# Kernel optimization log

Hardware: AMD Instinct MI355X
Metric: run time of the kernel (lower is better)

## Reference

```python
import jax, jax.numpy as jnp
import numpy as np

EMBED = 1024
HEADS = 16
HEAD_DIM = EMBED // HEADS
HIDDEN = 4 * EMBED
EPS = 1e-5


def setup_inputs() -> dict:
    key = jax.random.key(0)
    ks = jax.random.split(key, 9)
    s = lambda fan_in: 1.0 / np.sqrt(fan_in)
    inp = {
        "x": jax.random.normal(ks[0], (2, 2048, EMBED), dtype=jnp.float32),
        "ln1_w": jnp.ones((EMBED,), jnp.float32),
        "ln1_b": jnp.zeros((EMBED,), jnp.float32),
        "ln2_w": jnp.ones((EMBED,), jnp.float32),
        "ln2_b": jnp.zeros((EMBED,), jnp.float32),
        "qkv_w": jax.random.uniform(ks[1], (EMBED, 3 * EMBED), jnp.float32, -s(EMBED), s(EMBED)),
        "qkv_b": jax.random.uniform(ks[2], (3 * EMBED,), jnp.float32, -s(EMBED), s(EMBED)),
        "proj_w": jax.random.uniform(ks[3], (EMBED, EMBED), jnp.float32, -s(EMBED), s(EMBED)),
        "proj_b": jax.random.uniform(ks[4], (EMBED,), jnp.float32, -s(EMBED), s(EMBED)),
        "fc1_w": jax.random.uniform(ks[5], (EMBED, HIDDEN), jnp.float32, -s(EMBED), s(EMBED)),
        "fc1_b": jax.random.uniform(ks[6], (HIDDEN,), jnp.float32, -s(EMBED), s(EMBED)),
        "fc2_w": jax.random.uniform(ks[7], (HIDDEN, EMBED), jnp.float32, -s(HIDDEN), s(HIDDEN)),
        "fc2_b": jax.random.uniform(ks[8], (EMBED,), jnp.float32, -s(HIDDEN), s(HIDDEN)),
    }
    return inp


def _layernorm(x, w, b):
    mu = jnp.mean(x, axis=-1, keepdims=True)
    var = jnp.mean(jnp.square(x - mu), axis=-1, keepdims=True)
    return (x - mu) * jax.lax.rsqrt(var + EPS) * w + b


def _attn(x, qkv_w, qkv_b, proj_w, proj_b):
    B, N, C = x.shape
    qkv = x @ qkv_w + qkv_b                      # [B,N,3C]
    qkv = qkv.reshape(B, N, 3, HEADS, HEAD_DIM)
    q, k, v = qkv[:, :, 0], qkv[:, :, 1], qkv[:, :, 2]   # [B,N,H,D]
    scale = HEAD_DIM ** -0.5
    scores = jnp.einsum("bqhd,bkhd->bhqk", q, k) * scale  # [B,H,N,N]
    attn = jax.nn.softmax(scores, axis=-1)
    out = jnp.einsum("bhqk,bkhd->bqhd", attn, v).reshape(B, N, C)
    return out @ proj_w + proj_b


def _mlp(x, fc1_w, fc1_b, fc2_w, fc2_b):
    h = jax.nn.gelu(x @ fc1_w + fc1_b, approximate=False)
    return h @ fc2_w + fc2_b


def reference(x, ln1_w, ln1_b, ln2_w, ln2_b, qkv_w, qkv_b, proj_w, proj_b,
              fc1_w, fc1_b, fc2_w, fc2_b):
    # pre-norm transformer block (eval mode: dropout/drop_path are identity)
    x = x + _attn(_layernorm(x, ln1_w, ln1_b), qkv_w, qkv_b, proj_w, proj_b)
    x = x + _mlp(_layernorm(x, ln2_w, ln2_b), fc1_w, fc1_b, fc2_w, fc2_b)
    return x
```

## Files before the change

### kernel.cpp

```cpp
#include <hip/hip_runtime.h>
#include <hip/hip_bf16.h>

#define SEQ    2048
#define BATCH  2
#define MTOK   4096
#define EMBED  1024
#define HEADS  16
#define HDIM   64
#define QKV3   3072
#define FFN    4096

typedef __attribute__((ext_vector_type(8))) short bf16x8;
typedef __attribute__((ext_vector_type(4))) float f32x4;

static __device__ __forceinline__ unsigned short f2bf(float f) {
  union { float f; unsigned u; } x; x.f = f;
  unsigned r = x.u + 0x7FFFu + ((x.u >> 16) & 1u);
  return (unsigned short)(r >> 16);
}
static __device__ __forceinline__ float bf2f(unsigned short u) {
  union { unsigned u; float f; } x; x.u = ((unsigned)u) << 16; return x.f;
}
static __device__ __forceinline__ unsigned pk2bf(float a, float b) {
#if __has_builtin(__builtin_amdgcn_cvt_pk_bf16_f32)
  typedef __attribute__((ext_vector_type(2))) __bf16 bf16x2_t;
  union { bf16x2_t v; unsigned u; } x;
  x.v = __builtin_amdgcn_cvt_pk_bf16_f32(a, b);
  return x.u;
#else
  return ((unsigned)f2bf(a)) | (((unsigned)f2bf(b)) << 16);
#endif
}
static __device__ __forceinline__ float fexp2(float x) {
#if __has_builtin(__builtin_amdgcn_exp2f)
  return __builtin_amdgcn_exp2f(x);
#else
  return exp2f(x);
#endif
}

static __device__ __forceinline__ void gload16(const unsigned short* g, unsigned short* l) {
  __builtin_amdgcn_global_load_lds((const __attribute__((address_space(1))) void*)g,
                                   (__attribute__((address_space(3))) void*)l, 16, 0, 0);
}

struct TD { const float* W; unsigned short* T; int K, N, ntx, base; };
struct TD4 { TD d[4]; };

__global__ void transpose_all(TD4 td) {
  __shared__ float t[32][33];
  int bid = blockIdx.x;
  int i = 0;
  if (bid >= td.d[1].base) i = 1;
  if (bid >= td.d[2].base) i = 2;
  if (bid >= td.d[3].base) i = 3;
  const TD& D = td.d[i];
  int local = bid - D.base;
  int n0 = (local % D.ntx) * 32, k0 = (local / D.ntx) * 32;
  int tx = threadIdx.x, ty = threadIdx.y;
#pragma unroll
  for (int j = 0; j < 32; j += 8)
    t[ty + j][tx] = D.W[(size_t)(k0 + ty + j) * D.N + n0 + tx];
  __syncthreads();
#pragma unroll
  for (int j = 0; j < 32; j += 8)
    D.T[(size_t)(n0 + ty + j) * D.K + k0 + tx] = f2bf(t[tx][ty + j]);
}

__global__ __launch_bounds__(256) void ln_kernel(const float* __restrict__ in,
                                                 const float* __restrict__ w,
                                                 const float* __restrict__ b,
                                                 unsigned short* __restrict__ out) {
  __shared__ float sh[4];
  int row = blockIdx.x, tid = threadIdx.x;
  const float4 v = ((const float4*)(in + (size_t)row * EMBED))[tid];
  float s = v.x + v.y + v.z + v.w;
#pragma unroll
  for (int off = 32; off; off >>= 1) s += __shfl_xor(s, off);
  if ((tid & 63) == 0) sh[tid >> 6] = s;
  __syncthreads();
  float mean = (sh[0] + sh[1] + sh[2] + sh[3]) * (1.0f / EMBED);
  __syncthreads();
  float dx = v.x - mean, dy = v.y - mean, dz = v.z - mean, dw = v.w - mean;
  float q = dx * dx + dy * dy + dz * dz + dw * dw;
#pragma unroll
  for (int off = 32; off; off >>= 1) q += __shfl_xor(q, off);
  if ((tid & 63) == 0) sh[tid >> 6] = q;
  __syncthreads();
  float var = (sh[0] + sh[1] + sh[2] + sh[3]) * (1.0f / EMBED);
  float rs = rsqrtf(var + 1e-5f);
  const float4 wv = ((const float4*)w)[tid];
  const float4 bv = ((const float4*)b)[tid];
  ushort4 o;
  o.x = f2bf(dx * rs * wv.x + bv.x);
  o.y = f2bf(dy * rs * wv.y + bv.y);
  o.z = f2bf(dz * rs * wv.z + bv.z);
  o.w = f2bf(dw * rs * wv.w + bv.w);
  ((ushort4*)(out + (size_t)row * EMBED))[tid] = o;
}

template <int ACT, int OUTBF, int VSPLIT>
__global__ __launch_bounds__(256) void gemmBig(const unsigned short* __restrict__ A,
                                               const unsigned short* __restrict__ Wt,
                                               const float* __restrict__ bias,
                                               unsigned short* __restrict__ outB,
                                               float* __restrict__ outF,
                                               unsigned short* __restrict__ vT,
                                               int M, int N, int K, int nblk) {
  __shared__ __align__(16) unsigned short As[128 * 64];
  __shared__ __align__(16) unsigned short Bs[128 * 64];
  const int tid = threadIdx.x;
  const int wave = tid >> 6, lane = tid & 63;
  const int quad = lane >> 4, ml = lane & 15;
  const int wr = wave >> 1, wc = wave & 1;
  const int m0 = (blockIdx.x / nblk) * 128;
  const int n0 = (blockIdx.x % nblk) * 128;
  const int srow = lane >> 3;
  const int schunk = (lane & 7) ^ (srow & 7);
  const unsigned short* Ag = A + (size_t)(m0 + wave * 32 + srow) * K + schunk * 8;
  const unsigned short* Bg = Wt + (size_t)(n0 + wave * 32 + srow) * K + schunk * 8;
  unsigned short* AsW = &As[wave * 2048];
  unsigned short* BsW = &Bs[wave * 2048];
  f32x4 acc[4][4];
#pragma unroll
  for (int i = 0; i < 4; i++)
#pragma unroll
    for (int j = 0; j < 4; j++) acc[i][j] = (f32x4){0.f, 0.f, 0.f, 0.f};
  for (int k0 = 0; k0 < K; k0 += 64) {
    __syncthreads();
#pragma unroll
    for (int t = 0; t < 4; t++) {
      gload16(Ag + (size_t)(8 * t) * K, AsW + 512 * t);
      gload16(Bg + (size_t)(8 * t) * K, BsW + 512 * t);
    }
    Ag += 64; Bg += 64;
    __syncthreads();
#pragma unroll
    for (int kh = 0; kh < 2; kh++) {
      const int ch = ((kh * 4 + quad) ^ (ml & 7)) * 8;
      bf16x8 af[4], bfr[4];
#pragma unroll
      for (int mt = 0; mt < 4; mt++)
        af[mt] = *(const bf16x8*)&As[(wr * 64 + mt * 16 + ml) * 64 + ch];
#pragma unroll
      for (int nt = 0; nt < 4; nt++)
        bfr[nt] = *(const bf16x8*)&Bs[(wc * 64 + nt * 16 + ml) * 64 + ch];
#pragma unroll
      for (int mt = 0; mt < 4; mt++)
#pragma unroll
        for (int nt = 0; nt < 4; nt++)
          acc[mt][nt] = __builtin_amdgcn_mfma_f32_16x16x32_bf16(af[mt], bfr[nt], acc[mt][nt], 0, 0, 0);
    }
  }
#pragma unroll
  for (int mt = 0; mt < 4; mt++)
#pragma unroll
    for (int nt = 0; nt < 4; nt++) {
      const int col0 = n0 + wc * 64 + nt * 16;
      const int row0 = m0 + wr * 64 + mt * 16;
      if (VSPLIT && col0 >= 2 * EMBED) {
        const int b = row0 >> 11, tok0 = row0 & (SEQ - 1);
        const int h = (col0 - 2 * EMBED) >> 6;
        const int dl = ((col0 - 2 * EMBED) & 63) + ml;
        float bia = bias[col0 + ml];
        ushort4 o;
        o.x = f2bf(acc[mt][nt][0] + bia);
        o.y = f2bf(acc[mt][nt][1] + bia);
        o.z = f2bf(acc[mt][nt][2] + bia);
        o.w = f2bf(acc[mt][nt][3] + bia);
        *(ushort4*)(vT + (size_t)((b * 16 + h) * 64 + dl) * SEQ + tok0 + quad * 4) = o;
      } else {
#pragma unroll
        for (int r = 0; r < 4; r++) {
          int row = row0 + quad * 4 + r;
          int col = col0 + ml;
          float v = acc[mt][nt][r] + bias[col];
          if (ACT) v = 0.5f * v * (1.0f + erff(v * 0.70710678118f));
          if (OUTBF)
            outB[(size_t)row * N + col] = f2bf(v);
          else
            outF[(size_t)row * N + col] = v;
        }
      }
    }
}

template <int RES, int OUTBF>
__global__ __launch_bounds__(256) void gemm64k(const unsigned short* __restrict__ A,
                                               const unsigned short* __restrict__ Wt,
                                               const float* __restrict__ bias,
                                               const float* __restrict__ res,
                                               unsigned short* __restrict__ outB,
                                               float* __restrict__ outF,
                                               int M, int N, int K, int nblk) {
  __shared__ __align__(16) unsigned short As[128 * 64];
  __shared__ __align__(16) unsigned short Bs[64 * 64];
  const int tid = threadIdx.x;
  const int wave = tid >> 6, lane = tid & 63;
  const int quad = lane >> 4, ml = lane & 15;
  const int wr = wave >> 1, wc = wave & 1;
  const int xcd = blockIdx.x & 7, idx = blockIdx.x >> 3;
  const int mPerXcd = (gridDim.x >> 3) / nblk;
  const int m0 = (xcd * mPerXcd + idx / nblk) * 128;
  const int n0 = (idx % nblk) * 64;
  const int srow = lane >> 3;
  const int schunk = (lane & 7) ^ (srow & 7);
  const unsigned short* Ag = A + (size_t)(m0 + wave * 32 + srow) * K + schunk * 8;
  const unsigned short* Bg = Wt + (size_t)(n0 + wave * 16 + srow) * K + schunk * 8;
  unsigned short* AsW = &As[wave * 2048];
  unsigned short* BsW = &Bs[wave * 1024];
  f32x4 acc[4][2];
#pragma unroll
  for (int i = 0; i < 4; i++) { acc[i][0] = (f32x4){0.f,0.f,0.f,0.f}; acc[i][1] = acc[i][0]; }
  for (int k0 = 0; k0 < K; k0 += 64) {
    __syncthreads();
    gload16(Ag, AsW);
    gload16(Ag + (size_t)8 * K,  AsW + 512);
    gload16(Ag + (size_t)16 * K, AsW + 1024);
    gload16(Ag + (size_t)24 * K, AsW + 1536);
    gload16(Bg, BsW);
    gload16(Bg + (size_t)8 * K,  BsW + 512);
    Ag += 64; Bg += 64;
    __syncthreads();
#pragma unroll
    for (int kh = 0; kh < 2; kh++) {
      const int ch = ((kh * 4 + quad) ^ (ml & 7)) * 8;
      bf16x8 af[4], bfr[2];
#pragma unroll
      for (int mt = 0; mt < 4; mt++)
        af[mt] = *(const bf16x8*)&As[(wr * 64 + mt * 16 + ml) * 64 + ch];
#pragma unroll
      for (int nt = 0; nt < 2; nt++)
        bfr[nt] = *(const bf16x8*)&Bs[(wc * 32 + nt * 16 + ml) * 64 + ch];
#pragma unroll
      for (int mt = 0; mt < 4; mt++)
#pragma unroll
        for (int nt = 0; nt < 2; nt++)
          acc[mt][nt] = __builtin_amdgcn_mfma_f32_16x16x32_bf16(af[mt], bfr[nt], acc[mt][nt], 0, 0, 0);
    }
  }
#pragma unroll
  for (int mt = 0; mt < 4; mt++)
#pragma unroll
    for (int nt = 0; nt < 2; nt++)
#pragma unroll
      for (int r = 0; r < 4; r++) {
        int row = m0 + wr * 64 + mt * 16 + quad * 4 + r;
        int col = n0 + wc * 32 + nt * 16 + ml;
        float v = acc[mt][nt][r] + bias[col];
        if (RES) v += res[(size_t)row * N + col];
        if (OUTBF)
          outB[(size_t)row * N + col] = f2bf(v);
        else
          outF[(size_t)row * N + col] = v;
      }
}

__global__ __launch_bounds__(256) void attn_kernel(const unsigned short* __restrict__ qkv,
                                                   const unsigned short* __restrict__ vT,
                                                   unsigned short* __restrict__ attn) {
  __shared__ __align__(16) unsigned short Ks[2][64 * 64];
  __shared__ __align__(16) unsigned short Vs[2][64 * 64];
  __shared__ __align__(16) unsigned short Ps[4][16 * 64];
  const int tid = threadIdx.x, wave = tid >> 6, lane = tid & 63;
  const int quad = lane >> 4, ml = lane & 15;
  const int bh = blockIdx.x, b = bh >> 4, h = bh & 15;
  const int q0 = blockIdx.y * 64 + wave * 16;
  const float qscale = 0.18033688011112042f;
  const unsigned short* qrow = qkv + (size_t)(b * SEQ + q0 + ml) * QKV3 + h * HDIM;
  bf16x8 aq0 = *(const bf16x8*)(qrow + quad * 8);
  bf16x8 aq1 = *(const bf16x8*)(qrow + 32 + quad * 8);
#pragma unroll
  for (int j = 0; j < 8; j++) {
    aq0[j] = (short)f2bf(bf2f((unsigned short)aq0[j]) * qscale);
    aq1[j] = (short)f2bf(bf2f((unsigned short)aq1[j]) * qscale);
  }
  bf16x8 ones;
#pragma unroll
  for (int j = 0; j < 8; j++) ones[j] = (short)0x3F80;
  f32x4 O[4], lsum = {0.f, 0.f, 0.f, 0.f};
#pragma unroll
  for (int i = 0; i < 4; i++) O[i] = (f32x4){0.f, 0.f, 0.f, 0.f};
  const int skey = lane >> 3;
  const int schunk8 = (((lane & 7) ^ ((lane >> 3) & 7))) * 8;
  const int swz = (ml & 7);
  const unsigned short* kbase =
      qkv + (size_t)(b * SEQ + wave * 16 + skey) * QKV3 + EMBED + h * HDIM + schunk8;
  const unsigned short* vbase =
      vT + (size_t)(bh * 64 + wave * 16 + skey) * SEQ + schunk8;
  unsigned short* PsW = &Ps[wave][0];

  gload16(kbase, &Ks[0][wave * 1024]);
  gload16(kbase + (size_t)8 * QKV3, &Ks[0][wave * 1024] + 512);
  gload16(vbase, &Vs[0][wave * 1024]);
  gload16(vbase + (size_t)8 * SEQ, &Vs[0][wave * 1024] + 512);
  __syncthreads();

  for (int kti = 0; kti < SEQ / 64; ++kti) {
    const int cur = kti & 1;
    if (kti + 1 < SEQ / 64) {
      const int kt = (kti + 1) * 64;
      unsigned short* kd = &Ks[cur ^ 1][wave * 1024];
      unsigned short* vd = &Vs[cur ^ 1][wave * 1024];
      gload16(kbase + (size_t)kt * QKV3, kd);
      gload16(kbase + (size_t)(kt + 8) * QKV3, kd + 512);
      gload16(vbase + kt, vd);
      gload16(vbase + kt + (size_t)8 * SEQ, vd + 512);
    }
    const unsigned short* Kc = &Ks[cur][0];
    const unsigned short* Vc = &Vs[cur][0];
#pragma unroll
    for (int s = 0; s < 4; s++) {
      bf16x8 blo = *(const bf16x8*)&Kc[(s * 16 + ml) * 64 + (quad ^ swz) * 8];
      bf16x8 bhi = *(const bf16x8*)&Kc[(s * 16 + ml) * 64 + ((4 + quad) ^ swz) * 8];
      f32x4 St = {0.f, 0.f, 0.f, 0.f};
      St = __builtin_amdgcn_mfma_f32_16x16x32_bf16(blo, aq0, St, 0, 0, 0);
      St = __builtin_amdgcn_mfma_f32_16x16x32_bf16(bhi, aq1, St, 0, 0, 0);
      uint2 pk_;
      pk_.x = pk2bf(fexp2(St[0]), fexp2(St[1]));
      pk_.y = pk2bf(fexp2(St[2]), fexp2(St[3]));
      const int chs = (2 * s + (quad >> 1)) ^ swz;
      *(uint2*)((char*)PsW + ml * 128 + chs * 16 + (quad & 1) * 8) = pk_;
    }
    bf16x8 ap0 = *(const bf16x8*)((const char*)PsW + ml * 128 + ((quad ^ swz) << 4));
    bf16x8 ap1 = *(const bf16x8*)((const char*)PsW + ml * 128 + (((4 + quad) ^ swz) << 4));
    __builtin_amdgcn_s_setprio(1);
    lsum = __builtin_amdgcn_mfma_f32_16x16x32_bf16(ap0, ones, lsum, 0, 0, 0);
    lsum = __builtin_amdgcn_mfma_f32_16x16x32_bf16(ap1, ones, lsum, 0, 0, 0);
#pragma unroll
    for (int d = 0; d < 4; d++) {
      bf16x8 bv0 = *(const bf16x8*)&Vs[cur][(d * 16 + ml) * 64 + (quad ^ swz) * 8];
      bf16x8 bv1 = *(const bf16x8*)&Vc[(d * 16 + ml) * 64 + ((4 + quad) ^ swz) * 8];
      O[d] = __builtin_amdgcn_mfma_f32_16x16x32_bf16(ap0, bv0, O[d], 0, 0, 0);
      O[d] = __builtin_amdgcn_mfma_f32_16x16x32_bf16(ap1, bv1, O[d], 0, 0, 0);
    }
    __builtin_amdgcn_s_setprio(0);
    __syncthreads();
  }
#pragma unroll
  for (int r = 0; r < 4; r++) {
    float inv = 1.0f / lsum[r];
    size_t g = (size_t)(b * SEQ + q0 + quad * 4 + r) * EMBED + h * HDIM + ml;
    attn[g + 0]  = f2bf(O[0][r] * inv);
    attn[g + 16] = f2bf(O[1][r] * inv);
    attn[g + 32] = f2bf(O[2][r] * inv);
    attn[g + 48] = f2bf(O[3][r] * inv);
  }
}

extern "C" void kernel_launch(void* const* d_in, const int* in_sizes, int n_in,
                              void* d_out, int out_size, void* d_ws, size_t ws_size,
                              hipStream_t stream) {
  const float* x      = (const float*)d_in[0];
  const float* ln1_w  = (const float*)d_in[1];
  const float* ln1_b  = (const float*)d_in[2];
  const float* ln2_w  = (const float*)d_in[3];
  const float* ln2_b  = (const float*)d_in[4];
  const float* qkv_w  = (const float*)d_in[5];
  const float* qkv_b  = (const float*)d_in[6];
  const float* proj_w = (const float*)d_in[7];
  const float* proj_b = (const float*)d_in[8];
  const float* fc1_w  = (const float*)d_in[9];
  const float* fc1_b  = (const float*)d_in[10];
  const float* fc2_w  = (const float*)d_in[11];
  const float* fc2_b  = (const float*)d_in[12];
  float* out = (float*)d_out;
  char* wsb = (char*)d_ws;
  unsigned short* lnbuf  = (unsigned short*)(wsb + 0);
  unsigned short* qkvb   = (unsigned short*)(wsb + 8388608);
  unsigned short* attnb  = (unsigned short*)(wsb + 33554432);
  unsigned short* vTb    = (unsigned short*)(wsb + 41943040);
  unsigned short* actb   = (unsigned short*)(wsb + 33554432);
  float*          h1     = (float*)(wsb + 67108864);
  unsigned short* qkvWt  = (unsigned short*)(wsb + 83886080);
  unsigned short* projWt = (unsigned short*)(wsb + 90177536);
  unsigned short* fc1Wt  = (unsigned short*)(wsb + 92274688);
  unsigned short* fc2Wt  = (unsigned short*)(wsb + 100663296);

  TD4 td;
  td.d[0] = {qkv_w,  qkvWt,  1024, 3072,  96, 0};
  td.d[1] = {proj_w, projWt, 1024, 1024,  32, 3072};
  td.d[2] = {fc1_w,  fc1Wt,  1024, 4096, 128, 4096};
  td.d[3] = {fc2_w,  fc2Wt,  4096, 1024,  32, 8192};
  transpose_all<<<12288, dim3(32, 8), 0, stream>>>(td);

  ln_kernel<<<MTOK, 256, 0, stream>>>(x, ln1_w, ln1_b, lnbuf);
  gemmBig<0, 1, 1><<<768, 256, 0, stream>>>(
      lnbuf, qkvWt, qkv_b, qkvb, nullptr, vTb, MTOK, QKV3, EMBED, 24);
  attn_kernel<<<dim3(32, 32), 256, 0, stream>>>(qkvb, vTb, attnb);
  gemm64k<1, 0><<<512, 256, 0, stream>>>(
      attnb, projWt, proj_b, x, nullptr, h1, MTOK, EMBED, EMBED, 16);
  ln_kernel<<<MTOK, 256, 0, stream>>>(h1, ln2_w, ln2_b, lnbuf);
  gemmBig<1, 1, 0><<<1024, 256, 0, stream>>>(
      lnbuf, fc1Wt, fc1_b, actb, nullptr, nullptr, MTOK, FFN, EMBED, 32);
  gemm64k<1, 0><<<512, 256, 0, stream>>>(
      actb, fc2Wt, fc2_b, h1, nullptr, out, MTOK, EMBED, FFN, 16);
}
```

Measured before the change: 365.0 us.

## Double-buffer K-loop tiles in gemm64k and use fast sigmoid GELU approximation

Measured after the change: 348.6 us. 4.5% less time.

```diff
diff --git a/kernel.cpp b/kernel.cpp
--- a/kernel.cpp
+++ b/kernel.cpp
@@ -37,6 +37,18 @@
 #else
   return exp2f(x);
 #endif
+}
+static __device__ __forceinline__ float frcp(float x) {
+#if __has_builtin(__builtin_amdgcn_rcpf)
+  return __builtin_amdgcn_rcpf(x);
+#else
+  return 1.0f / x;
+#endif
+}
+static __device__ __forceinline__ float fgelu(float v) {
+  float t = v * v;
+  float z = v * __builtin_fmaf(-0.1029456f, t, -2.3022650687f);
+  return v * frcp(1.0f + fexp2(z));
 }
 
 static __device__ __forceinline__ void gload16(const unsigned short* g, unsigned short* l) {
@@ -175,7 +187,7 @@
           int row = row0 + quad * 4 + r;
           int col = col0 + ml;
           float v = acc[mt][nt][r] + bias[col];
-          if (ACT) v = 0.5f * v * (1.0f + erff(v * 0.70710678118f));
+          if (ACT) v = fgelu(v);
           if (OUTBF)
             outB[(size_t)row * N + col] = f2bf(v);
           else
@@ -193,8 +205,8 @@
                                                unsigned short* __restrict__ outB,
                                                float* __restrict__ outF,
                                                int M, int N, int K, int nblk) {
-  __shared__ __align__(16) unsigned short As[128 * 64];
-  __shared__ __align__(16) unsigned short Bs[64 * 64];
+  __shared__ __align__(16) unsigned short As[2][128 * 64];
+  __shared__ __align__(16) unsigned short Bs[2][64 * 64];
   const int tid = threadIdx.x;
   const int wave = tid >> 6, lane = tid & 63;
   const int quad = lane >> 4, ml = lane & 15;
@@ -207,13 +219,12 @@
   const int schunk = (lane & 7) ^ (srow & 7);
   const unsigned short* Ag = A + (size_t)(m0 + wave * 32 + srow) * K + schunk * 8;
   const unsigned short* Bg = Wt + (size_t)(n0 + wave * 16 + srow) * K + schunk * 8;
-  unsigned short* AsW = &As[wave * 2048];
-  unsigned short* BsW = &Bs[wave * 1024];
   f32x4 acc[4][2];
 #pragma unroll
   for (int i = 0; i < 4; i++) { acc[i][0] = (f32x4){0.f,0.f,0.f,0.f}; acc[i][1] = acc[i][0]; }
-  for (int k0 = 0; k0 < K; k0 += 64) {
-    __syncthreads();
+  {
+    unsigned short* AsW = &As[0][wave * 2048];
+    unsigned short* BsW = &Bs[0][wave * 1024];
     gload16(Ag, AsW);
     gload16(Ag + (size_t)8 * K,  AsW + 512);
     gload16(Ag + (size_t)16 * K, AsW + 1024);
@@ -221,23 +232,39 @@
     gload16(Bg, BsW);
     gload16(Bg + (size_t)8 * K,  BsW + 512);
     Ag += 64; Bg += 64;
-    __syncthreads();
+  }
+  __syncthreads();
+  const int nk = K >> 6;
+  for (int kk = 0; kk < nk; ++kk) {
+    const int cur = kk & 1;
+    if (kk + 1 < nk) {
+      unsigned short* AsW = &As[cur ^ 1][wave * 2048];
+      unsigned short* BsW = &Bs[cur ^ 1][wave * 1024];
+      gload16(Ag, AsW);
+      gload16(Ag + (size_t)8 * K,  AsW + 512);
+      gload16(Ag + (size_t)16 * K, AsW + 1024);
+      gload16(Ag + (size_t)24 * K, AsW + 1536);
+      gload16(Bg, BsW);
+      gload16(Bg + (size_t)8 * K,  BsW + 512);
+      Ag += 64; Bg += 64;
+    }
 #pragma unroll
     for (int kh = 0; kh < 2; kh++) {
       const int ch = ((kh * 4 + quad) ^ (ml & 7)) * 8;
       bf16x8 af[4], bfr[2];
 #pragma unroll
       for (int mt = 0; mt < 4; mt++)
-        af[mt] = *(const bf16x8*)&As[(wr * 64 + mt * 16 + ml) * 64 + ch];
+        af[mt] = *(const bf16x8*)&As[cur][(wr * 64 + mt * 16 + ml) * 64 + ch];
 #pragma unroll
       for (int nt = 0; nt < 2; nt++)
-        bfr[nt] = *(const bf16x8*)&Bs[(wc * 32 + nt * 16 + ml) * 64 + ch];
+        bfr[nt] = *(const bf16x8*)&Bs[cur][(wc * 32 + nt * 16 + ml) * 64 + ch];
 #pragma unroll
       for (int mt = 0; mt < 4; mt++)
 #pragma unroll
         for (int nt = 0; nt < 2; nt++)
           acc[mt][nt] = __builtin_amdgcn_mfma_f32_16x16x32_bf16(af[mt], bfr[nt], acc[mt][nt], 0, 0, 0);
     }
+    __syncthreads();
   }
 #pragma unroll
   for (int mt = 0; mt < 4; mt++)
@@ -329,7 +356,7 @@
     lsum = __builtin_amdgcn_mfma_f32_16x16x32_bf16(ap1, ones, lsum, 0, 0, 0);
 #pragma unroll
     for (int d = 0; d < 4; d++) {
-      bf16x8 bv0 = *(const bf16x8*)&Vs[cur][(d * 16 + ml) * 64 + (quad ^ swz) * 8];
+      bf16x8 bv0 = *(const bf16x8*)&Vc[(d * 16 + ml) * 64 + (quad ^ swz) * 8];
       bf16x8 bv1 = *(const bf16x8*)&Vc[(d * 16 + ml) * 64 + ((4 + quad) ^ swz) * 8];
       O[d] = __builtin_amdgcn_mfma_f32_16x16x32_bf16(ap0, bv0, O[d], 0, 0, 0);
       O[d] = __builtin_amdgcn_mfma_f32_16x16x32_bf16(ap1, bv1, O[d], 0, 0, 0);
```
